# Kernel tuning notes

Hardware: AMD Instinct MI355X
Metric: run time of the kernel (lower is better)

## Reference

```python
import jax, jax.numpy as jnp
import numpy as np

MAX_DISP = 2  # 5x5x5 = 125 shifts


def conv3d(x, w, b):
    # x: [N,C,D,H,W], w: [O,I,3,3,3], padding 1 == SAME for stride 1
    y = jax.lax.conv_general_dilated(x, w, (1, 1, 1), 'SAME',
                                     dimension_numbers=('NCDHW', 'OIDHW', 'NCDHW'))
    return y + b[None, :, None, None, None]


def _warp_one(vol, flw):
    # vol: [C,H,W,D], flw: [3,H,W,D]; trilinear sampling at grid+flow, border-clamped
    C, H, W, D = vol.shape
    gz, gy, gx = jnp.meshgrid(jnp.arange(H, dtype=jnp.float32),
                              jnp.arange(W, dtype=jnp.float32),
                              jnp.arange(D, dtype=jnp.float32), indexing='ij')
    z = gz + flw[0]; y = gy + flw[1]; x = gx + flw[2]
    z0f, y0f, x0f = jnp.floor(z), jnp.floor(y), jnp.floor(x)
    wz, wy, wx = z - z0f, y - y0f, x - x0f
    z0 = jnp.clip(z0f, 0, H - 1).astype(jnp.int32)
    z1 = jnp.clip(z0f + 1, 0, H - 1).astype(jnp.int32)
    y0 = jnp.clip(y0f, 0, W - 1).astype(jnp.int32)
    y1 = jnp.clip(y0f + 1, 0, W - 1).astype(jnp.int32)
    x0 = jnp.clip(x0f, 0, D - 1).astype(jnp.int32)
    x1 = jnp.clip(x0f + 1, 0, D - 1).astype(jnp.int32)
    out = jnp.zeros_like(vol)
    for zi, wzi in ((z0, 1.0 - wz), (z1, wz)):
        for yi, wyi in ((y0, 1.0 - wy), (y1, wy)):
            for xi, wxi in ((x0, 1.0 - wx), (x1, wx)):
                out = out + vol[:, zi, yi, xi] * (wzi * wyi * wxi)[None]
    return out


warp = jax.vmap(_warp_one)


def compute_cost_volume(f1, f2, max_disp):
    B, C, H, W, D = f1.shape
    f2p = jnp.pad(f2, ((0, 0), (0, 0), (max_disp, max_disp), (max_disp, max_disp), (max_disp, max_disp)))
    n = 2 * max_disp + 1
    cost = []
    for i in range(n):
        for j in range(n):
            for k in range(n):
                cost.append(jnp.mean(f1 * f2p[:, :, i:H + i, j:W + j, k:D + k], axis=1, keepdims=True))
    return jnp.concatenate(cost, axis=1)  # [B,125,H,W,D]


def reference(moving, fixed, flow, context, w0, b0, w1, b1, w2, b2, w3, b3, w4, b4):
    shape = moving.shape[2:]
    up_context = jax.image.resize(context, context.shape[:2] + shape, method='trilinear')
    warped = warp(moving, flow)
    # normalize_features(normalize=True, center=True, across_channels=True, across_images=True)
    axes = (1, 2, 3, 4)
    m = 0.5 * (jnp.mean(warped, axes, keepdims=True) + jnp.mean(fixed, axes, keepdims=True))
    s = 0.5 * (jnp.std(warped, axis=axes, ddof=1, keepdims=True) +
               jnp.std(fixed, axis=axes, ddof=1, keepdims=True))
    warped_n = (warped - m) / s
    fixed_n = (fixed - m) / s
    cv = jax.nn.leaky_relu(compute_cost_volume(fixed_n, warped_n, MAX_DISP), 0.05)
    x_in = jnp.concatenate([up_context, flow, cv, fixed], axis=1)  # 32+3+125+16 = 176 ch
    ws = [w0, w1, w2, w3]
    bs = [b0, b1, b2, b3]
    x_out = x_in
    for w, b in zip(ws, bs):
        x_out = jax.nn.leaky_relu(conv3d(x_in, w, b), 0.02)
        x_in = jnp.concatenate([x_in, x_out], axis=1)
    context_out = x_out
    refinement = conv3d(context_out, w4, b4)
    return context_out, flow + refinement


def setup_inputs() -> dict:
    key = jax.random.key(0)
    ks = jax.random.split(key, 16)
    B, C, S = 1, 16, 48
    inp = {
        'moving': jax.random.normal(ks[0], (B, C, S, S, S), jnp.float32),
        'fixed': jax.random.normal(ks[1], (B, C, S, S, S), jnp.float32),
        'flow': jax.random.normal(ks[2], (B, 3, S, S, S), jnp.float32),
        'context': jax.random.normal(ks[3], (B, 32, S // 2, S // 2, S // 2), jnp.float32),
    }
    chans_in = [176, 240, 288, 320, 16]
    chans_out = [64, 48, 32, 16, 3]
    for i, (ci, co) in enumerate(zip(chans_in, chans_out)):
        inp[f'w{i}'] = 0.02 * jax.random.normal(ks[4 + i], (co, ci, 3, 3, 3), jnp.float32)
        inp[f'b{i}'] = jnp.zeros((co,), jnp.float32)
    return inp
```

## Files before the change

kernel.cpp:

```cpp
#include <hip/hip_runtime.h>
#include <cstddef>

#define SD 48
#define VOX (SD*SD*SD)
#define CSD 24
#define CVOL (CSD*CSD*CSD)
#define CST 352
#define PPL 2500
#define XPBYTES 88000000ull

typedef __attribute__((ext_vector_type(8))) short short8v;
typedef __attribute__((ext_vector_type(4))) short short4v;
typedef __attribute__((ext_vector_type(4))) float float4v;

__device__ __forceinline__ float lrelu(float x, float a){ return x > 0.f ? x : a*x; }

__device__ __forceinline__ unsigned short f2bf(float f){
    unsigned u = __float_as_uint(f);
    unsigned r = (u + 0x7fffu + ((u >> 16) & 1u)) >> 16;
    return (unsigned short)r;
}
__device__ __forceinline__ float bf2f(unsigned short s){
    return __uint_as_float(((unsigned)s) << 16);
}
__device__ __forceinline__ unsigned pk2(float a, float b){
    return (unsigned)f2bf(a) | ((unsigned)f2bf(b) << 16);
}

__device__ __forceinline__ void decode(int v, int &i, int &j, int &k){
    i = v / (SD*SD);
    int r = v - i*(SD*SD);
    j = r / SD;
    k = r - j*SD;
}

__global__ __launch_bounds__(256) void k_shell(unsigned short* __restrict__ Xp){
    int v = blockIdx.x*256 + threadIdx.x;
    if (v >= 125000) return;
    int pz = v / 2500, r = v % 2500, py = r / 50, px = r % 50;
    if (pz==0||pz==49||py==0||py==49||px==0||px==49){
        uint4* p = (uint4*)(Xp + (size_t)v*CST);
        uint4 zz = make_uint4(0,0,0,0);
        #pragma unroll
        for (int g=0; g<44; g++) p[g] = zz;
    }
}

__global__ __launch_bounds__(256) void k_warp_prep(
        const float* __restrict__ moving, const float* __restrict__ fixd,
        const float* __restrict__ flow, const float* __restrict__ context,
        unsigned short* __restrict__ WARPB, float* __restrict__ part,
        unsigned short* __restrict__ Xp)
{
    int v = blockIdx.x*256 + threadIdx.x;
    int i,j,k; decode(v,i,j,k);
    size_t pvox = (size_t)((i+1)*PPL + (j+1)*50 + (k+1))*CST;

    float f0 = flow[v], f1 = flow[VOX+v], f2v = flow[2*VOX+v];
    float z = (float)i + f0;
    float y = (float)j + f1;
    float x = (float)k + f2v;
    float z0f=floorf(z), y0f=floorf(y), x0f=floorf(x);
    float wz=z-z0f, wy=y-y0f, wx=x-x0f;
    int z0=min(max((int)z0f,0),SD-1), z1=min(max((int)z0f+1,0),SD-1);
    int y0=min(max((int)y0f,0),SD-1), y1=min(max((int)y0f+1,0),SD-1);
    int x0=min(max((int)x0f,0),SD-1), x1=min(max((int)x0f+1,0),SD-1);
    int b000=(z0*SD+y0)*SD+x0, b001=(z0*SD+y0)*SD+x1;
    int b010=(z0*SD+y1)*SD+x0, b011=(z0*SD+y1)*SD+x1;
    int b100=(z1*SD+y0)*SD+x0, b101=(z1*SD+y0)*SD+x1;
    int b110=(z1*SD+y1)*SD+x0, b111=(z1*SD+y1)*SD+x1;
    float w000=(1.f-wz)*(1.f-wy)*(1.f-wx), w001=(1.f-wz)*(1.f-wy)*wx;
    float w010=(1.f-wz)*wy*(1.f-wx),       w011=(1.f-wz)*wy*wx;
    float w100=wz*(1.f-wy)*(1.f-wx),       w101=wz*(1.f-wy)*wx;
    float w110=wz*wy*(1.f-wx),             w111=wz*wy*wx;

    float ow[16];
    float sw=0.f, ssw=0.f, sf=0.f, ssf=0.f;
    #pragma unroll
    for (int c=0;c<16;c++){
        const float* mc = moving + (size_t)c*VOX;
        float o = mc[b000]*w000 + mc[b001]*w001 + mc[b010]*w010 + mc[b011]*w011
                + mc[b100]*w100 + mc[b101]*w101 + mc[b110]*w110 + mc[b111]*w111;
        ow[c] = o;
        sw += o; ssw += o*o;
        float f = fixd[(size_t)c*VOX+v];
        sf += f; ssf += f*f;
    }
    uint4 q0 = make_uint4(pk2(ow[0],ow[1]), pk2(ow[2],ow[3]), pk2(ow[4],ow[5]), pk2(ow[6],ow[7]));
    uint4 q1 = make_uint4(pk2(ow[8],ow[9]), pk2(ow[10],ow[11]), pk2(ow[12],ow[13]), pk2(ow[14],ow[15]));
    uint4* wp = (uint4*)(WARPB + (size_t)v*16);
    wp[0] = q0; wp[1] = q1;

    float zc=0.5f*(float)i-0.25f, yc=0.5f*(float)j-0.25f, xc=0.5f*(float)k-0.25f;
    float cz0f=floorf(zc), cy0f=floorf(yc), cx0f=floorf(xc);
    float cwz=zc-cz0f, cwy=yc-cy0f, cwx=xc-cx0f;
    int cz0=min(max((int)cz0f,0),CSD-1), cz1=min(max((int)cz0f+1,0),CSD-1);
    int cy0=min(max((int)cy0f,0),CSD-1), cy1=min(max((int)cy0f+1,0),CSD-1);
    int cx0=min(max((int)cx0f,0),CSD-1), cx1=min(max((int)cx0f+1,0),CSD-1);
    int c000=(cz0*CSD+cy0)*CSD+cx0, c001=(cz0*CSD+cy0)*CSD+cx1;
    int c010=(cz0*CSD+cy1)*CSD+cx0, c011=(cz0*CSD+cy1)*CSD+cx1;
    int c100=(cz1*CSD+cy0)*CSD+cx0, c101=(cz1*CSD+cy0)*CSD+cx1;
    int c110=(cz1*CSD+cy1)*CSD+cx0, c111=(cz1*CSD+cy1)*CSD+cx1;
    float u000=(1.f-cwz)*(1.f-cwy)*(1.f-cwx), u001=(1.f-cwz)*(1.f-cwy)*cwx;
    float u010=(1.f-cwz)*cwy*(1.f-cwx),       u011=(1.f-cwz)*cwy*cwx;
    float u100=cwz*(1.f-cwy)*(1.f-cwx),       u101=cwz*(1.f-cwy)*cwx;
    float u110=cwz*cwy*(1.f-cwx),             u111=cwz*cwy*cwx;

    float oc[32];
    #pragma unroll
    for (int c=0;c<32;c++){
        const float* cc = context + (size_t)c*CVOL;
        oc[c] = cc[c000]*u000 + cc[c001]*u001 + cc[c010]*u010 + cc[c011]*u011
              + cc[c100]*u100 + cc[c101]*u101 + cc[c110]*u110 + cc[c111]*u111;
    }
    uint4* dst = (uint4*)(Xp + pvox);
    #pragma unroll
    for (int g=0; g<4; g++)
        dst[g] = make_uint4(pk2(oc[g*8+0],oc[g*8+1]), pk2(oc[g*8+2],oc[g*8+3]),
                            pk2(oc[g*8+4],oc[g*8+5]), pk2(oc[g*8+6],oc[g*8+7]));
    *(unsigned*)(Xp + pvox + 32) = pk2(f0, f1);
    Xp[pvox + 34] = f2bf(f2v);
    float fx[16];
    #pragma unroll
    for (int c=0;c<16;c++) fx[c] = fixd[(size_t)c*VOX+v];
    uint4* dstF = (uint4*)(Xp + pvox + 160);
    dstF[0] = make_uint4(pk2(fx[0],fx[1]),  pk2(fx[2],fx[3]),  pk2(fx[4],fx[5]),  pk2(fx[6],fx[7]));
    dstF[1] = make_uint4(pk2(fx[8],fx[9]),  pk2(fx[10],fx[11]),pk2(fx[12],fx[13]),pk2(fx[14],fx[15]));

    __shared__ float4 red[256];
    int tid=threadIdx.x;
    red[tid] = make_float4(sw,ssw,sf,ssf);
    __syncthreads();
    for (int off=128; off>0; off>>=1){
        if (tid<off){
            float4 a=red[tid], b2=red[tid+off];
            red[tid]=make_float4(a.x+b2.x, a.y+b2.y, a.z+b2.z, a.w+b2.w);
        }
        __syncthreads();
    }
    if (tid==0){
        float4 r=red[0];
        part[blockIdx.x]       = r.x;
        part[432+blockIdx.x]   = r.y;
        part[864+blockIdx.x]   = r.z;
        part[1296+blockIdx.x]  = r.w;
    }
}

__global__ __launch_bounds__(256) void k_stats(const float* __restrict__ part,
                                               float* __restrict__ stats)
{
    int tid=threadIdx.x;
    double acc[4]={0,0,0,0};
    for (int i=tid;i<432;i+=256){
        acc[0]+=part[i]; acc[1]+=part[432+i]; acc[2]+=part[864+i]; acc[3]+=part[1296+i];
    }
    __shared__ double red[256];
    double res[4]={0,0,0,0};
    for (int q=0;q<4;q++){
        red[tid]=acc[q]; __syncthreads();
        for (int off=128;off>0;off>>=1){
            if (tid<off) red[tid]+=red[tid+off];
            __syncthreads();
        }
        res[q]=red[0];
        __syncthreads();
    }
    if (tid==0){
        double N = 16.0*(double)VOX;
        double mw = res[0]/N, mf = res[2]/N;
        double vw = (res[1] - res[0]*res[0]/N)/(N-1.0);
        double vf = (res[3] - res[2]*res[2]/N)/(N-1.0);
        double m = 0.5*(mw+mf);
        double s = 0.5*(sqrt(vw)+sqrt(vf));
        stats[0]=(float)m;
        stats[1]=(float)(1.0/s);
    }
}

__global__ __launch_bounds__(256) void k_cv(
        const float* __restrict__ fixd, const unsigned short* __restrict__ WARPB,
        const float* __restrict__ stats, unsigned short* __restrict__ Xp)
{
    int v = blockIdx.x*256 + threadIdx.x;
    int i,j,k; decode(v,i,j,k);
    size_t pvox = (size_t)((i+1)*PPL + (j+1)*50 + (k+1))*CST;
    float m = stats[0], inv_s = stats[1];
    float fn[16]; float sfn = 0.f;
    #pragma unroll
    for (int c=0;c<16;c++){ fn[c] = (fixd[(size_t)c*VOX+v]-m)*inv_s; sfn += fn[c]; }
    float scale = inv_s*(1.0f/16.0f);
    float msfn = m*sfn;

    float res[125];
    #pragma unroll
    for (int dz=-2;dz<=2;dz++){
        int zz=i+dz;
        #pragma unroll
        for (int dy=-2;dy<=2;dy++){
            int yy=j+dy;
            #pragma unroll
            for (int dx=-2;dx<=2;dx++){
                int xx=k+dx;
                const int r = (dz+2)*25+(dy+2)*5+(dx+2);
                float o = 0.f;
                if ((unsigned)zz<SD && (unsigned)yy<SD && (unsigned)xx<SD){
                    int vs=(zz*SD+yy)*SD+xx;
                    const short8v* wr = (const short8v*)(WARPB + (size_t)vs*16);
                    short8v wlo = wr[0], whi = wr[1];
                    float d = 0.f;
                    #pragma unroll
                    for (int e=0;e<8;e++) d += fn[e]   * bf2f((unsigned short)wlo[e]);
                    #pragma unroll
                    for (int e=0;e<8;e++) d += fn[8+e] * bf2f((unsigned short)whi[e]);
                    o = lrelu(scale*(d - msfn), 0.05f);
                }
                res[r] = o;
            }
        }
    }
    Xp[pvox + 35] = f2bf(res[0]);
    {
        short4v s4;
        #pragma unroll
        for (int e=0;e<4;e++) s4[e] = (short)f2bf(res[1+e]);
        *(short4v*)(Xp + pvox + 36) = s4;
    }
    #pragma unroll
    for (int g=0; g<15; g++){
        short8v s8;
        #pragma unroll
        for (int e=0;e<8;e++) s8[e] = (short)f2bf(res[5+g*8+e]);
        *(short8v*)(Xp + pvox + 40 + g*8) = s8;
    }
}

__global__ __launch_bounds__(256) void k_wb(
        const float* __restrict__ w, unsigned short* __restrict__ dst,
        int CO, int CIN, int CT, int total)
{
    int idx = blockIdx.x*256 + threadIdx.x;
    if (idx >= total) return;
    int e = idx & 7;
    int l = (idx >> 3) & 63;
    int rest = idx >> 9;
    int ct = rest % CT;
    int rest2 = rest / CT;
    int tn = rest2 % 27;
    int chunk = rest2 / 27;
    int dz = tn/9, rr = tn%9, dxx = rr/3, dyy = rr%3;
    int t_orig = dz*9 + dyy*3 + dxx;
    int co = ct*16 + (l & 15);
    int cin = chunk*32 + (l >> 4)*8 + e;
    unsigned short v = 0;
    if (co < CO && cin < CIN) v = f2bf(w[((size_t)co*CIN + cin)*27 + t_orig]);
    dst[idx] = v;
}

template<int CT, int DEPTH, int MODE>
__global__ __launch_bounds__(128) void k_mconv(
        const unsigned short* __restrict__ Xp,
        const unsigned short* __restrict__ Wb,
        const float* __restrict__ bias,
        int nchunks, int ch_base,
        unsigned short* __restrict__ Ydst,
        float* __restrict__ outf,
        const float* __restrict__ flw)
{
    __shared__ unsigned short slab[13824];
    const int tid = threadIdx.x;
    const int bid0 = blockIdx.x;
    const int bid = (bid0 & 7)*108 + (bid0 >> 3);
    const int xt = bid % 3, yt = (bid/3) % 12, zt = bid / 36;
    const int x0 = xt*16, y0 = yt*4, z0 = zt*2;
    const int lane = tid & 63, w = tid >> 6;
    const int lx = lane & 15, kb = lane >> 4;

    int voff[14];
    #pragma unroll
    for (int i=0;i<14;i++){
        int u = tid + i*128;
        int p = u >> 2, q = u & 3;
        int sx = p % 18; int pr = p / 18; int sy = pr % 6; int sz = pr / 6;
        sz = min(sz, 3);
        voff[i] = ((z0+sz)*PPL + (y0+sy)*50 + (x0+sx))*CST + q*8;
    }

    float4v acc[4][CT];
    #pragma unroll
    for (int vt=0; vt<4; vt++)
        #pragma unroll
        for (int ct=0; ct<CT; ct++)
            acc[vt][ct] = (float4v){0.f,0.f,0.f,0.f};

    const unsigned short* wl = Wb + (size_t)lane*8;
    const int gmax = nchunks*27 - 1;
    short8v a[DEPTH][CT];
    #pragma unroll
    for (int d=0; d<DEPTH-1; d++)
        #pragma unroll
        for (int ct=0; ct<CT; ct++)
            a[d][ct] = *(const short8v*)(wl + (size_t)min(d,gmax)*(CT*512) + (size_t)ct*512);

    for (int chunk=0; chunk<nchunks; chunk++){
        const int cb = ch_base + chunk*32;
        __syncthreads();
        #pragma unroll
        for (int i=0;i<14;i++){
            int u = tid + i*128;
            if (i < 13 || u < 1728){
                const unsigned short* g = Xp + voff[i] + cb;
                __builtin_amdgcn_global_load_lds(
                    (const __attribute__((address_space(1))) void*)g,
                    (__attribute__((address_space(3))) void*)(slab + (size_t)u*8),
                    16, 0, 0);
            }
        }
        __syncthreads();

        const int gb = chunk*27;
        #pragma unroll
        for (int dz=0; dz<3; dz++){
            #pragma unroll
            for (int dxx=0; dxx<3; dxx++){
                short8v brow[6];
                #pragma unroll
                for (int yi=0; yi<6; yi++)
                    brow[yi] = *(const short8v*)(slab
                        + (size_t)((((w+dz)*6 + yi)*18 + dxx + lx)*32 + kb*8));
                #pragma unroll
                for (int dyy=0; dyy<3; dyy++){
                    const int t = dz*9 + dxx*3 + dyy;
                    {
                        int g2 = gb + t + (DEPTH-1); g2 = min(g2, gmax);
                        #pragma unroll
                        for (int ct=0; ct<CT; ct++)
                            a[(t+DEPTH-1)%DEPTH][ct] = *(const short8v*)(wl
                                + (size_t)g2*(CT*512) + (size_t)ct*512);
                    }
                    __builtin_amdgcn_s_setprio(1);
                    #pragma unroll
                    for (int vt=0; vt<4; vt++)
                        #pragma unroll
                        for (int ct=0; ct<CT; ct++)
                            acc[vt][ct] = __builtin_amdgcn_mfma_f32_16x16x32_bf16(
                                              a[t%DEPTH][ct], brow[vt+dyy], acc[vt][ct], 0, 0, 0);
                    __builtin_amdgcn_s_setprio(0);
                }
            }
        }
    }

    const int x = x0 + lx, z = z0 + w;
    #pragma unroll
    for (int vt=0; vt<4; vt++){
        const int y = y0 + vt;
        const size_t pvox = (size_t)((z+1)*PPL + (y+1)*50 + (x+1))*CST;
        const int vi = (z*SD + y)*SD + x;
        #pragma unroll
        for (int ct=0; ct<CT; ct++){
            if (MODE == 2){
                #pragma unroll
                for (int r=0; r<4; r++){
                    const int co = ct*16 + kb*4 + r;
                    if (co < 3){
                        float vv = acc[vt][ct][r] + bias[co];
                        outf[(size_t)co*VOX + vi] = flw[(size_t)co*VOX + vi] + vv;
                    }
                }
            } else {
                const int co0 = ct*16 + kb*4;
                short4v s4;
                #pragma unroll
                for (int r=0; r<4; r++){
                    float vv = acc[vt][ct][r] + bias[co0+r];
                    float o = lrelu(vv, 0.02f);
                    s4[r] = (short)f2bf(o);
                    if (MODE == 1)
                        outf[(size_t)(co0+r)*VOX + vi] = o;
                }
                *(short4v*)(Ydst + pvox + co0) = s4;
            }
        }
    }
}

extern "C" void kernel_launch(void* const* d_in, const int* in_sizes, int n_in,
                              void* d_out, int out_size, void* d_ws, size_t ws_size,
                              hipStream_t stream) {
    const float* moving  = (const float*)d_in[0];
    const float* fixd    = (const float*)d_in[1];
    const float* flow    = (const float*)d_in[2];
    const float* context = (const float*)d_in[3];
    const float* w0 = (const float*)d_in[4];  const float* b0 = (const float*)d_in[5];
    const float* w1 = (const float*)d_in[6];  const float* b1 = (const float*)d_in[7];
    const float* w2 = (const float*)d_in[8];  const float* b2 = (const float*)d_in[9];
    const float* w3 = (const float*)d_in[10]; const float* b3 = (const float*)d_in[11];
    const float* w4 = (const float*)d_in[12]; const float* b4 = (const float*)d_in[13];

    char* ws = (char*)d_ws;
    unsigned short* Xp    = (unsigned short*)ws;
    unsigned short* WARPB = (unsigned short*)(ws + XPBYTES);
    float* PART  = (float*)(ws + XPBYTES + 3538944ull);
    float* STATS = (float*)(ws + XPBYTES + 3538944ull + 8192ull);
    unsigned short* Wb0 = (unsigned short*)(ws + XPBYTES + 3538944ull + 9216ull);
    unsigned short* Wb1 = Wb0 + (size_t)331776;
    unsigned short* Wb2 = Wb1 + (size_t)331776;
    unsigned short* Wb3 = Wb2 + (size_t)248832;
    unsigned short* Wb4 = Wb3 + (size_t)138240;

    float* ctx_out  = (float*)d_out;
    float* flow_out = (float*)d_out + (size_t)16*VOX;

    k_shell<<<489,256,0,stream>>>(Xp);
    k_warp_prep<<<432,256,0,stream>>>(moving, fixd, flow, context, WARPB, PART, Xp);
    k_stats<<<1,256,0,stream>>>(PART, STATS);
    k_cv<<<432,256,0,stream>>>(fixd, WARPB, STATS, Xp);

    int n0 = 6*27*4*512;   k_wb<<<(n0+255)/256,256,0,stream>>>(w0, Wb0, 64, 176, 4, n0);
    int n1 = 8*27*3*512;   k_wb<<<(n1+255)/256,256,0,stream>>>(w1, Wb1, 48, 240, 3, n1);
    int n2 = 9*27*2*512;   k_wb<<<(n2+255)/256,256,0,stream>>>(w2, Wb2, 32, 288, 2, n2);
    int n3 = 10*27*1*512;  k_wb<<<(n3+255)/256,256,0,stream>>>(w3, Wb3, 16, 320, 1, n3);
    int n4 = 1*27*1*512;   k_wb<<<(n4+255)/256,256,0,stream>>>(w4, Wb4,  3,  16, 1, n4);

    k_mconv<4,3,0><<<864,128,0,stream>>>(Xp, Wb0, b0, 6,  0,   Xp+176, nullptr, nullptr);
    k_mconv<3,3,0><<<864,128,0,stream>>>(Xp, Wb1, b1, 8,  0,   Xp+240, nullptr, nullptr);
    k_mconv<2,9,0><<<864,128,0,stream>>>(Xp, Wb2, b2, 9,  0,   Xp+288, nullptr, nullptr);
    k_mconv<1,9,1><<<864,128,0,stream>>>(Xp, Wb3, b3, 10, 0,   Xp+320, ctx_out, nullptr);
    k_mconv<1,3,2><<<864,128,0,stream>>>(Xp, Wb4, b4, 1,  320, Xp,     flow_out, flow);
}
```

Measured before the change: 400.1 us.

## Add LDS-staged conv kernel with weight prefetch; merge prep and weight-repack launches

Introduces k_mconv_g for the first two conv layers. It stages each 32-channel input slab into LDS with global_load_lds and reuses six LDS rows across the three dy taps. It also double-buffers the per-tap weight fragments in registers and raises wave priority around the MFMA bursts. Separately, the padding-shell zeroing is folded into extra blocks of k_warp_prep, and the five weight-repack launches are merged into one kernel. Together these aim to cut launch overhead and hide global load latency in the heaviest conv layers, at the cost of more registers per thread, which may lower occupancy.

```diff
diff --git a/kernel.cpp b/kernel.cpp
--- a/kernel.cpp
+++ b/kernel.cpp
@@ -34,24 +34,25 @@
     k = r - j*SD;
 }
 
-__global__ __launch_bounds__(256) void k_shell(unsigned short* __restrict__ Xp){
-    int v = blockIdx.x*256 + threadIdx.x;
-    if (v >= 125000) return;
-    int pz = v / 2500, r = v % 2500, py = r / 50, px = r % 50;
-    if (pz==0||pz==49||py==0||py==49||px==0||px==49){
-        uint4* p = (uint4*)(Xp + (size_t)v*CST);
-        uint4 zz = make_uint4(0,0,0,0);
-        #pragma unroll
-        for (int g=0; g<44; g++) p[g] = zz;
-    }
-}
-
 __global__ __launch_bounds__(256) void k_warp_prep(
         const float* __restrict__ moving, const float* __restrict__ fixd,
         const float* __restrict__ flow, const float* __restrict__ context,
         unsigned short* __restrict__ WARPB, float* __restrict__ part,
         unsigned short* __restrict__ Xp)
 {
+    if (blockIdx.x >= 432){
+        int v = (blockIdx.x - 432)*256 + threadIdx.x;
+        if (v < 125000){
+            int pz = v / 2500, r = v % 2500, py = r / 50, px = r % 50;
+            if (pz==0||pz==49||py==0||py==49||px==0||px==49){
+                uint4* p = (uint4*)(Xp + (size_t)v*CST);
+                uint4 zz = make_uint4(0,0,0,0);
+                #pragma unroll
+                for (int g=0; g<44; g++) p[g] = zz;
+            }
+        }
+        return;
+    }
     int v = blockIdx.x*256 + threadIdx.x;
     int i,j,k; decode(v,i,j,k);
     size_t pvox = (size_t)((i+1)*PPL + (j+1)*50 + (k+1))*CST;
@@ -235,12 +236,9 @@
     }
 }
 
-__global__ __launch_bounds__(256) void k_wb(
-        const float* __restrict__ w, unsigned short* __restrict__ dst,
-        int CO, int CIN, int CT, int total)
-{
-    int idx = blockIdx.x*256 + threadIdx.x;
-    if (idx >= total) return;
+__device__ __forceinline__ void wb_one(int idx, const float* __restrict__ w,
+        unsigned short* __restrict__ dst, int CO, int CIN, int CT)
+{
     int e = idx & 7;
     int l = (idx >> 3) & 63;
     int rest = idx >> 9;
@@ -255,6 +253,27 @@
     unsigned short v = 0;
     if (co < CO && cin < CIN) v = f2bf(w[((size_t)co*CIN + cin)*27 + t_orig]);
     dst[idx] = v;
+}
+
+__global__ __launch_bounds__(256) void k_wb_all(
+        const float* __restrict__ w0, const float* __restrict__ w1,
+        const float* __restrict__ w2, const float* __restrict__ w3,
+        const float* __restrict__ w4,
+        unsigned short* __restrict__ Wb0, unsigned short* __restrict__ Wb1,
+        unsigned short* __restrict__ Wb2, unsigned short* __restrict__ Wb3,
+        unsigned short* __restrict__ Wb4)
+{
+    const int n0=331776, n1=331776, n2=248832, n3=138240, n4=13824;
+    int idx = blockIdx.x*256 + threadIdx.x;
+    if (idx < n0){ wb_one(idx, w0, Wb0, 64, 176, 4); return; }
+    idx -= n0;
+    if (idx < n1){ wb_one(idx, w1, Wb1, 48, 240, 3); return; }
+    idx -= n1;
+    if (idx < n2){ wb_one(idx, w2, Wb2, 32, 288, 2); return; }
+    idx -= n2;
+    if (idx < n3){ wb_one(idx, w3, Wb3, 16, 320, 1); return; }
+    idx -= n3;
+    if (idx < n4){ wb_one(idx, w4, Wb4,  3,  16, 1); return; }
 }
 
 template<int CT, int DEPTH, int MODE>
@@ -385,6 +404,128 @@
     }
 }
 
+template<int CT, int MODE>
+__global__ __launch_bounds__(128) void k_mconv_g(
+        const unsigned short* __restrict__ Xp,
+        const unsigned short* __restrict__ Wb,
+        const float* __restrict__ bias,
+        int nchunks, int ch_base,
+        unsigned short* __restrict__ Ydst,
+        float* __restrict__ outf)
+{
+    __shared__ unsigned short slab[13824];
+    const int tid = threadIdx.x;
+    const int bid0 = blockIdx.x;
+    const int bid = (bid0 & 7)*108 + (bid0 >> 3);
+    const int xt = bid % 3, yt = (bid/3) % 12, zt = bid / 36;
+    const int x0 = xt*16, y0 = yt*4, z0 = zt*2;
+    const int lane = tid & 63, w = tid >> 6;
+    const int lx = lane & 15, kb = lane >> 4;
+
+    int voff[14];
+    #pragma unroll
+    for (int i=0;i<14;i++){
+        int u = tid + i*128;
+        int p = u >> 2, q = u & 3;
+        int sx = p % 18; int pr = p / 18; int sy = pr % 6; int sz = pr / 6;
+        sz = min(sz, 3);
+        voff[i] = ((z0+sz)*PPL + (y0+sy)*50 + (x0+sx))*CST + q*8;
+    }
+
+    float4v acc[4][CT];
+    #pragma unroll
+    for (int vt=0; vt<4; vt++)
+        #pragma unroll
+        for (int ct=0; ct<CT; ct++)
+            acc[vt][ct] = (float4v){0.f,0.f,0.f,0.f};
+
+    const unsigned short* wl = Wb + (size_t)lane*8;
+    const int ggmax = nchunks*9 - 1;
+    short8v cur[3][CT], nxt[3][CT];
+    #pragma unroll
+    for (int j=0; j<3; j++)
+        #pragma unroll
+        for (int ct=0; ct<CT; ct++)
+            cur[j][ct] = *(const short8v*)(wl + (size_t)j*(CT*512) + (size_t)ct*512);
+
+    for (int chunk=0; chunk<nchunks; chunk++){
+        const int cb = ch_base + chunk*32;
+        __syncthreads();
+        #pragma unroll
+        for (int i=0;i<14;i++){
+            int u = tid + i*128;
+            if (i < 13 || u < 1728){
+                const unsigned short* g = Xp + voff[i] + cb;
+                __builtin_amdgcn_global_load_lds(
+                    (const __attribute__((address_space(1))) void*)g,
+                    (__attribute__((address_space(3))) void*)(slab + (size_t)u*8),
+                    16, 0, 0);
+            }
+        }
+        __syncthreads();
+
+        #pragma unroll
+        for (int dz=0; dz<3; dz++){
+            #pragma unroll
+            for (int dxx=0; dxx<3; dxx++){
+                const int g = dz*3 + dxx;
+                {
+                    int ggn = min(chunk*9 + g + 1, ggmax);
+                    #pragma unroll
+                    for (int j=0; j<3; j++)
+                        #pragma unroll
+                        for (int ct=0; ct<CT; ct++)
+                            nxt[j][ct] = *(const short8v*)(wl
+                                + ((size_t)ggn*3 + j)*(CT*512) + (size_t)ct*512);
+                }
+                short8v brow[6];
+                #pragma unroll
+                for (int yi=0; yi<6; yi++)
+                    brow[yi] = *(const short8v*)(slab
+                        + (size_t)((((w+dz)*6 + yi)*18 + dxx + lx)*32 + kb*8));
+                #pragma unroll
+                for (int dyy=0; dyy<3; dyy++){
+                    __builtin_amdgcn_s_setprio(1);
+                    #pragma unroll
+                    for (int vt=0; vt<4; vt++)
+                        #pragma unroll
+                        for (int ct=0; ct<CT; ct++)
+                            acc[vt][ct] = __builtin_amdgcn_mfma_f32_16x16x32_bf16(
+                                              cur[dyy][ct], brow[vt+dyy], acc[vt][ct], 0, 0, 0);
+                    __builtin_amdgcn_s_setprio(0);
+                }
+                #pragma unroll
+                for (int j=0; j<3; j++)
+                    #pragma unroll
+                    for (int ct=0; ct<CT; ct++)
+                        cur[j][ct] = nxt[j][ct];
+            }
+        }
+    }
+
+    const int x = x0 + lx, z = z0 + w;
+    #pragma unroll
+    for (int vt=0; vt<4; vt++){
+        const int y = y0 + vt;
+        const size_t pvox = (size_t)((z+1)*PPL + (y+1)*50 + (x+1))*CST;
+        const int vi = (z*SD + y)*SD + x;
+        #pragma unroll
+        for (int ct=0; ct<CT; ct++){
+            const int co0 = ct*16 + kb*4;
+            short4v s4;
+            #pragma unroll
+            for (int r=0; r<4; r++){
+                float vv = acc[vt][ct][r] + bias[co0+r];
+                float o = lrelu(vv, 0.02f);
+                s4[r] = (short)f2bf(o);
+                if (MODE == 1)
+                    outf[(size_t)(co0+r)*VOX + vi] = o;
+            }
+            *(short4v*)(Ydst + pvox + co0) = s4;
+        }
+    }
+}
+
 extern "C" void kernel_launch(void* const* d_in, const int* in_sizes, int n_in,
                               void* d_out, int out_size, void* d_ws, size_t ws_size,
                               hipStream_t stream) {
@@ -412,19 +553,13 @@
     float* ctx_out  = (float*)d_out;
     float* flow_out = (float*)d_out + (size_t)16*VOX;
 
-    k_shell<<<489,256,0,stream>>>(Xp);
-    k_warp_prep<<<432,256,0,stream>>>(moving, fixd, flow, context, WARPB, PART, Xp);
+    k_warp_prep<<<921,256,0,stream>>>(moving, fixd, flow, context, WARPB, PART, Xp);
     k_stats<<<1,256,0,stream>>>(PART, STATS);
     k_cv<<<432,256,0,stream>>>(fixd, WARPB, STATS, Xp);
-
-    int n0 = 6*27*4*512;   k_wb<<<(n0+255)/256,256,0,stream>>>(w0, Wb0, 64, 176, 4, n0);
-    int n1 = 8*27*3*512;   k_wb<<<(n1+255)/256,256,0,stream>>>(w1, Wb1, 48, 240, 3, n1);
-    int n2 = 9*27*2*512;   k_wb<<<(n2+255)/256,256,0,stream>>>(w2, Wb2, 32, 288, 2, n2);
-    int n3 = 10*27*1*512;  k_wb<<<(n3+255)/256,256,0,stream>>>(w3, Wb3, 16, 320, 1, n3);
-    int n4 = 1*27*1*512;   k_wb<<<(n4+255)/256,256,0,stream>>>(w4, Wb4,  3,  16, 1, n4);
-
-    k_mconv<4,3,0><<<864,128,0,stream>>>(Xp, Wb0, b0, 6,  0,   Xp+176, nullptr, nullptr);
-    k_mconv<3,3,0><<<864,128,0,stream>>>(Xp, Wb1, b1, 8,  0,   Xp+240, nullptr, nullptr);
+    k_wb_all<<<4158,256,0,stream>>>(w0, w1, w2, w3, w4, Wb0, Wb1, Wb2, Wb3, Wb4);
+
+    k_mconv_g<4,0><<<864,128,0,stream>>>(Xp, Wb0, b0, 6,  0,   Xp+176, nullptr);
+    k_mconv_g<3,0><<<864,128,0,stream>>>(Xp, Wb1, b1, 8,  0,   Xp+240, nullptr);
     k_mconv<2,9,0><<<864,128,0,stream>>>(Xp, Wb2, b2, 9,  0,   Xp+288, nullptr, nullptr);
     k_mconv<1,9,1><<<864,128,0,stream>>>(Xp, Wb3, b3, 10, 0,   Xp+320, ctx_out, nullptr);
     k_mconv<1,3,2><<<864,128,0,stream>>>(Xp, Wb4, b4, 1,  320, Xp,     flow_out, flow);
```

Result: no change. 406.9 us (+1.7%).
